# Kernel optimization log

Hardware: AMD Instinct MI355X
Metric: run time of the kernel (lower is better)

## Reference

```python
import jax, jax.numpy as jnp
import numpy as np

B, N, M, D, CD, H, DH = 2, 2048, 2048, 1024, 1024, 8, 64
INNER = H * DH  # 512
FFD = 4 * D
SCALE = DH ** -0.5


def _ln(x, g, b):
    mu = jnp.mean(x, axis=-1, keepdims=True)
    var = jnp.mean((x - mu) ** 2, axis=-1, keepdims=True)
    return (x - mu) * jax.lax.rsqrt(var + 1e-5) * g + b


def _ff(x, g, b, w1, b1, w2, b2):
    h = jax.nn.gelu(_ln(x, g, b) @ w1 + b1, approximate=False)
    return h @ w2 + b2


def setup_inputs() -> dict:
    key = jax.random.key(0)
    ks = jax.random.split(key, 16)
    s = 0.02
    return {
        'x': jax.random.normal(ks[0], (B, N, D), jnp.float32),
        'context': jax.random.normal(ks[1], (B, M, CD), jnp.float32),
        'mask': jnp.ones((B, N), bool),
        'context_mask': jnp.ones((B, M), bool),
        'ln_x_g': jnp.ones(D), 'ln_x_b': jnp.zeros(D),
        'ln_c_g': jnp.ones(CD), 'ln_c_b': jnp.zeros(CD),
        'W_qk': jax.random.normal(ks[2], (D, INNER)) * s,
        'W_v': jax.random.normal(ks[3], (D, INNER)) * s,
        'Wc_qk': jax.random.normal(ks[4], (CD, INNER)) * s,
        'Wc_v': jax.random.normal(ks[5], (CD, INNER)) * s,
        'W_out': jax.random.normal(ks[6], (INNER, D)) * s, 'b_out': jnp.zeros(D),
        'Wc_out': jax.random.normal(ks[7], (INNER, CD)) * s, 'bc_out': jnp.zeros(CD),
        'ff_g': jnp.ones(D), 'ff_b': jnp.zeros(D),
        'ff_w1': jax.random.normal(ks[8], (D, FFD)) * s, 'ff_b1': jnp.zeros(FFD),
        'ff_w2': jax.random.normal(ks[9], (FFD, D)) * s, 'ff_b2': jnp.zeros(D),
        'cff_g': jnp.ones(CD), 'cff_b': jnp.zeros(CD),
        'cff_w1': jax.random.normal(ks[10], (CD, FFD)) * s, 'cff_b1': jnp.zeros(FFD),
        'cff_w2': jax.random.normal(ks[11], (FFD, CD)) * s, 'cff_b2': jnp.zeros(CD),
    }


def reference(x, context, mask, context_mask,
              ln_x_g, ln_x_b, ln_c_g, ln_c_b,
              W_qk, W_v, Wc_qk, Wc_v, W_out, b_out, Wc_out, bc_out,
              ff_g, ff_b, ff_w1, ff_b1, ff_w2, ff_b2,
              cff_g, cff_b, cff_w1, cff_b1, cff_w2, cff_b2):
    # pre-norm bidirectional cross attention
    xn = _ln(x, ln_x_g, ln_x_b)
    cn = _ln(context, ln_c_g, ln_c_b)
    qk = (xn @ W_qk).reshape(B, N, H, DH)      # b i h d
    v = (xn @ W_v).reshape(B, N, H, DH)
    cqk = (cn @ Wc_qk).reshape(B, M, H, DH)    # b j h d
    cv = (cn @ Wc_v).reshape(B, M, H, DH)
    sim = jnp.einsum('bihd,bjhd->bhij', qk, cqk) * SCALE
    pair_mask = mask[:, None, :, None] & context_mask[:, None, None, :]
    big_neg = jnp.finfo(sim.dtype).max
    sim = jnp.where(pair_mask, sim, -big_neg)
    attn = jax.nn.softmax(sim, axis=-1)        # x attends over context (j)
    cattn = jax.nn.softmax(sim, axis=-2)       # context attends over x (i)
    out = jnp.einsum('bhij,bjhd->bihd', attn, cv).reshape(B, N, INNER)
    cout = jnp.einsum('bhij,bihd->bjhd', cattn, v).reshape(B, M, INNER)
    x = x + (out @ W_out + b_out)
    context = context + (cout @ Wc_out + bc_out)
    # dual pre-norm FFN residual
    x = _ff(x, ff_g, ff_b, ff_w1, ff_b1, ff_w2, ff_b2) + x
    context = _ff(context, cff_g, cff_b, cff_w1, cff_b1, cff_w2, cff_b2) + context
    return (x, context)
```

## Files before the change

kernel.cpp:

```cpp
#include <hip/hip_runtime.h>
#include <hip/hip_bf16.h>
#include <cmath>

typedef __hip_bfloat16 bf16;
typedef __attribute__((ext_vector_type(8))) short short8;
typedef __attribute__((ext_vector_type(4))) float f32x4;

#define B_     2
#define N_     2048
#define M_     2048
#define D_     1024
#define H_     8
#define DH_    64
#define INNER_ 512
#define FFD_   4096
#define ROWS   4096

__device__ __forceinline__ float b2f(bf16 x){ return __bfloat162float(x); }
__device__ __forceinline__ bf16  f2b(float x){ return __float2bfloat16(x); }
__device__ __forceinline__ float s2f(short s){
    unsigned u = ((unsigned)(unsigned short)s) << 16;
    float f; __builtin_memcpy(&f, &u, 4); return f;
}
__device__ __forceinline__ short f2s(float f){
    bf16 b = __float2bfloat16(f);
    short s; __builtin_memcpy(&s, &b, 2); return s;
}
__device__ __forceinline__ float ldx(const void* p, size_t i, bool isb){
    return isb ? __bfloat162float(((const bf16*)p)[i]) : ((const float*)p)[i];
}
__device__ __forceinline__ void stx(void* p, size_t i, float v, bool isb){
    if (isb) ((bf16*)p)[i] = f2b(v); else ((float*)p)[i] = v;
}
__device__ __forceinline__ void gld16(const bf16* g, bf16* l){
    __builtin_amdgcn_global_load_lds(
        (const __attribute__((address_space(1))) void*)g,
        (__attribute__((address_space(3))) void*)l, 16, 0, 0);
}
__device__ __forceinline__ short8 ds_read128(const bf16* p){
    unsigned a = (unsigned)(size_t)(const __attribute__((address_space(3))) bf16*)p;
    short8 r;
    asm volatile("ds_read_b128 %0, %1" : "=v"(r) : "v"(a));
    return r;
}

__global__ void probe_kernel(const void* ones, int* flag){
    unsigned w = *(const unsigned*)ones;
    *flag = (w == 0x3F803F80u) ? 1 : 0;
}

template<bool IN_EXT>
__global__ __launch_bounds__(256) void ln_kernel(const void* __restrict__ x,
    const void* __restrict__ g, const void* __restrict__ b,
    bf16* __restrict__ out, const int* __restrict__ flagp)
{
    const int C = 1024;
    bool f = (*flagp != 0);
    bool bx = IN_EXT ? f : true;
    size_t base = (size_t)blockIdx.x * C;
    int t = threadIdx.x;
    float v[4]; float s = 0.f;
#pragma unroll
    for (int q = 0; q < 4; q++){ v[q] = ldx(x, base + t + q*256, bx); s += v[q]; }
    __shared__ float red[256];
    red[t] = s; __syncthreads();
    for (int o = 128; o > 0; o >>= 1){ if (t < o) red[t] += red[t+o]; __syncthreads(); }
    float mu = red[0] * (1.0f/1024.0f);
    __syncthreads();
    s = 0.f;
#pragma unroll
    for (int q = 0; q < 4; q++){ float d = v[q]-mu; s += d*d; }
    red[t] = s; __syncthreads();
    for (int o = 128; o > 0; o >>= 1){ if (t < o) red[t] += red[t+o]; __syncthreads(); }
    float rstd = rsqrtf(red[0]*(1.0f/1024.0f) + 1e-5f);
    bf16* orow = out + base;
#pragma unroll
    for (int q = 0; q < 4; q++){
        int i = t + q*256;
        orow[i] = f2b((v[q]-mu)*rstd*ldx(g,i,f) + ldx(b,i,f));
    }
}

__global__ __launch_bounds__(256) void tcast_kernel(
    const void* __restrict__ in, bf16* __restrict__ out,
    int R, int Ccols, size_t ibs, size_t obs, int force_b16,
    const int* __restrict__ flagp)
{
    bool isb = force_b16 ? true : (*flagp != 0);
    __shared__ float T[32][33];
    size_t ib = (size_t)blockIdx.z * ibs, ob = (size_t)blockIdx.z * obs;
    int r0 = blockIdx.x * 32, c0 = blockIdx.y * 32;
    int tx = threadIdx.x & 31, ty = threadIdx.x >> 5;
#pragma unroll
    for (int rr = 0; rr < 32; rr += 8)
        T[ty + rr][tx] = ldx(in, ib + (size_t)(r0 + ty + rr) * Ccols + c0 + tx, isb);
    __syncthreads();
#pragma unroll
    for (int rr = 0; rr < 32; rr += 8)
        out[ob + (size_t)(c0 + ty + rr) * R + r0 + tx] = f2b(T[tx][ty + rr]);
}

template<int MODE, int EPI, int DP>
__global__ __launch_bounds__(256) void mfma_gemm(
    const bf16* __restrict__ A, const bf16* __restrict__ A2,
    const bf16* __restrict__ Bt,
    const void* __restrict__ bias, const void* __restrict__ bias2,
    const void* __restrict__ res,  const void* __restrict__ res2,
    void* __restrict__ C, void* __restrict__ C2,
    int K, int lda, int ldb, int ldc,
    size_t coff, size_t cstr, size_t roff, float scale, int bh0,
    int azdiv, size_t astr, size_t bstr, int zsplit,
    const int* __restrict__ flagp)
{
    __shared__ __align__(16) bf16 As[DP][128*32];
    __shared__ __align__(16) bf16 Bs[DP][128*32];
    const int t = threadIdx.x;
    const int wave = t >> 6, lane = t & 63;
    const int quad = lane >> 4, l16 = lane & 15;
    const int z = blockIdx.z;

    const bf16* Ab; const bf16* Bb;
    const void* biasp = bias; const void* resp = res; void* Cp = C;
    size_t cbase;
    if (MODE == 1){
        int bh = bh0 + z, b = bh >> 3, h = bh & 7;
        Ab = A + (size_t)b * N_ * lda + h * DH_ + (size_t)blockIdx.y * 128 * lda;
        Bb = Bt + (size_t)b * M_ * ldb + h * DH_ + (size_t)blockIdx.x * 128 * ldb;
        cbase = coff + (size_t)z * N_ * M_;
    } else {
        const bf16* Ause = A;
        if (z >= zsplit){
            if (A2)    Ause  = A2;
            if (bias2) biasp = bias2;
            if (res2)  resp  = res2;
            if (C2)    Cp    = C2;
        }
        Ab = Ause + (size_t)(z / azdiv) * astr + (size_t)blockIdx.y * 128 * lda;
        Bb = Bt + (size_t)z * bstr + (size_t)blockIdx.x * 128 * ldb;
        cbase = coff + (size_t)z * cstr;
    }

    const int c1 = t, c2 = t + 256;
    const int r1 = c1 >> 2, q1 = ((c1 & 3) - (r1 >> 1)) & 3;
    const int r2 = c2 >> 2, q2 = ((c2 & 3) - (r2 >> 1)) & 3;
    const bf16* ga1 = Ab + (size_t)r1 * lda + q1 * 8;
    const bf16* ga2 = Ab + (size_t)r2 * lda + q2 * 8;
    const bf16* gb1 = Bb + (size_t)r1 * ldb + q1 * 8;
    const bf16* gb2 = Bb + (size_t)r2 * ldb + q2 * 8;
    const int la1 = (wave * 64) * 8;
    const int la2 = (256 + wave * 64) * 8;
    const int moff = (wave & 1) * 64, noff = (wave >> 1) * 64;

    auto stage = [&](int d, int k0){
        gld16(ga1 + k0, &As[d][la1]);
        gld16(ga2 + k0, &As[d][la2]);
        gld16(gb1 + k0, &Bs[d][la1]);
        gld16(gb2 + k0, &Bs[d][la2]);
    };

    f32x4 acc[4][4];
#pragma unroll
    for (int mi = 0; mi < 4; mi++)
#pragma unroll
        for (int ni = 0; ni < 4; ni++)
#pragma unroll
            for (int r = 0; r < 4; r++) acc[mi][ni][r] = 0.f;

    const int nt = K >> 5;
    for (int d = 0; d < DP - 1; ++d)
        if (d < nt) stage(d, d * 32);

    for (int tt = 0; tt < nt; ++tt){
        if (tt + DP - 1 < nt) stage((tt + DP - 1) % DP, (tt + DP - 1) * 32);
        int rem = nt - 1 - tt;
        int lv  = rem < DP - 1 ? rem : DP - 1;
        if      (lv >= 3) asm volatile("s_waitcnt vmcnt(12)" ::: "memory");
        else if (lv == 2) asm volatile("s_waitcnt vmcnt(8)"  ::: "memory");
        else if (lv == 1) asm volatile("s_waitcnt vmcnt(4)"  ::: "memory");
        else              asm volatile("s_waitcnt vmcnt(0)"  ::: "memory");
        __builtin_amdgcn_s_barrier();
        const bf16* Al = As[tt % DP];
        const bf16* Bl = Bs[tt % DP];
        short8 af[4], bf8[4];
#pragma unroll
        for (int mi = 0; mi < 4; mi++){
            int rr = moff + mi*16 + l16;
            int qp = (quad + (rr >> 1)) & 3;
            af[mi] = ds_read128(Al + ((size_t)rr*4 + qp)*8);
        }
#pragma unroll
        for (int ni = 0; ni < 4; ni++){
            int rr = noff + ni*16 + l16;
            int qp = (quad + (rr >> 1)) & 3;
            bf8[ni] = ds_read128(Bl + ((size_t)rr*4 + qp)*8);
        }
        asm volatile("s_waitcnt lgkmcnt(0)" ::: "memory");
        __builtin_amdgcn_sched_barrier(0);
        __builtin_amdgcn_s_setprio(1);
#pragma unroll
        for (int mi = 0; mi < 4; mi++)
#pragma unroll
            for (int ni = 0; ni < 4; ni++)
                acc[mi][ni] = __builtin_amdgcn_mfma_f32_16x16x32_bf16(
                    af[mi], bf8[ni], acc[mi][ni], 0, 0, 0);
        __builtin_amdgcn_s_setprio(0);
        __builtin_amdgcn_s_barrier();
    }

    bool f = false;
    if (EPI >= 1) f = (*flagp != 0);
    const int mb = blockIdx.y * 128, nb = blockIdx.x * 128;
#pragma unroll
    for (int ni = 0; ni < 4; ni++){
        int n = nb + noff + ni*16 + l16;
        float bv = (EPI >= 1) ? ldx(biasp, n, f) : 0.0f;
#pragma unroll
        for (int mi = 0; mi < 4; mi++){
#pragma unroll
            for (int r = 0; r < 4; r++){
                int m = mb + moff + mi*16 + quad*4 + r;
                float val = acc[mi][ni][r] * scale + bv;
                if (EPI == 2) val = 0.5f*val*(1.0f + erff(val*0.70710678118f));
                size_t idx = (size_t)m * ldc + n;
                if (EPI == 3) val += ldx(resp, roff + idx, f);
                if (EPI == 4) val += b2f(((const bf16*)resp)[roff + idx]);
                if (EPI == 4) stx(Cp, cbase + idx, val, f);
                else ((bf16*)Cp)[cbase + idx] = f2b(val);
            }
        }
    }
}

__global__ __launch_bounds__(256) void flash_attn(
    const bf16* __restrict__ qk, const bf16* __restrict__ cqk,
    const bf16* __restrict__ vT, const bf16* __restrict__ cvT,
    bf16* __restrict__ aout, bf16* __restrict__ acout)
{
    __shared__ __align__(16) bf16 QP[64*72];
    __shared__ __align__(16) bf16 Ks[64*72];
    __shared__ __align__(16) bf16 Vs[64*72];
    const int t = threadIdx.x;
    const int wave = t >> 6, lane = t & 63, quad = lane >> 4, l16 = lane & 15;
    const int z = blockIdx.y;
    const int dir = z >> 4, bh = z & 15, b = bh >> 3, h = bh & 7;
    const bf16 *Qg, *Kg, *Vg; bf16* Og;
    if (dir == 0){ Qg = qk;  Kg = cqk; Vg = cvT; Og = aout;  }
    else         { Qg = cqk; Kg = qk;  Vg = vT;  Og = acout; }
    const int i0 = blockIdx.x * 64;
    const bf16* Qb = Qg + ((size_t)b*2048 + i0)*INNER_ + h*DH_;
    const bf16* Kb = Kg + (size_t)b*2048*INNER_ + h*DH_;
    const bf16* Vb = Vg + ((size_t)b*INNER_ + h*DH_)*2048;

    for (int c = t; c < 64*8; c += 256){
        int r = c >> 3, jc = c & 7;
        short8 raw = *(const short8*)(Qb + (size_t)r*INNER_ + jc*8);
        short8 s;
#pragma unroll
        for (int q = 0; q < 8; q++) s[q] = f2s(s2f(raw[q]) * 0.125f);
        *(short8*)(QP + r*72 + jc*8) = s;
    }
    __syncthreads();
    const int moff = wave * 16;
    short8 qf[2];
#pragma unroll
    for (int ks = 0; ks < 2; ks++){
        int rr = moff + l16;
        qf[ks] = *(const short8*)(QP + rr*72 + ks*32 + quad*8);
    }
    __syncthreads();

    f32x4 O[4];
    float mrow[4], lrow[4];
#pragma unroll
    for (int nd = 0; nd < 4; nd++)
#pragma unroll
        for (int r = 0; r < 4; r++) O[nd][r] = 0.f;
#pragma unroll
    for (int r = 0; r < 4; r++){ mrow[r] = -1e30f; lrow[r] = 0.f; }

    for (int j0 = 0; j0 < 2048; j0 += 64){
        for (int c = t; c < 64*8; c += 256){
            int r = c >> 3, jc = c & 7;
            short8 kraw = *(const short8*)(Kb + (size_t)(j0 + r)*INNER_ + jc*8);
            *(short8*)(Ks + r*72 + jc*8) = kraw;
            short8 vraw = *(const short8*)(Vb + (size_t)r*2048 + j0 + jc*8);
            *(short8*)(Vs + r*72 + jc*8) = vraw;
        }
        __syncthreads();
        f32x4 S[4];
#pragma unroll
        for (int ni = 0; ni < 4; ni++)
#pragma unroll
            for (int r = 0; r < 4; r++) S[ni][r] = 0.f;
#pragma unroll
        for (int ks = 0; ks < 2; ks++){
            short8 kf[4];
#pragma unroll
            for (int ni = 0; ni < 4; ni++){
                int rr = ni*16 + l16;
                kf[ni] = *(const short8*)(Ks + rr*72 + ks*32 + quad*8);
            }
#pragma unroll
            for (int ni = 0; ni < 4; ni++)
                S[ni] = __builtin_amdgcn_mfma_f32_16x16x32_bf16(
                    qf[ks], kf[ni], S[ni], 0, 0, 0);
        }
        float al[4];
#pragma unroll
        for (int r = 0; r < 4; r++){
            float rm = fmaxf(fmaxf(S[0][r], S[1][r]), fmaxf(S[2][r], S[3][r]));
#pragma unroll
            for (int d = 1; d < 16; d <<= 1)
                rm = fmaxf(rm, __shfl_xor(rm, d, 64));
            float mn = fmaxf(mrow[r], rm);
            al[r] = __expf(mrow[r] - mn);
            mrow[r] = mn;
        }
#pragma unroll
        for (int r = 0; r < 4; r++){
            float rs = 0.f;
#pragma unroll
            for (int ni = 0; ni < 4; ni++){
                float pv = __expf(S[ni][r] - mrow[r]);
                S[ni][r] = pv; rs += pv;
            }
#pragma unroll
            for (int d = 1; d < 16; d <<= 1)
                rs += __shfl_xor(rs, d, 64);
            lrow[r] = lrow[r]*al[r] + rs;
        }
#pragma unroll
        for (int nd = 0; nd < 4; nd++)
#pragma unroll
            for (int r = 0; r < 4; r++) O[nd][r] *= al[r];
#pragma unroll
        for (int ni = 0; ni < 4; ni++)
#pragma unroll
            for (int r = 0; r < 4; r++){
                int row = moff + quad*4 + r;
                QP[row*72 + ni*16 + l16] = f2b(S[ni][r]);
            }
        __syncthreads();
#pragma unroll
        for (int ks = 0; ks < 2; ks++){
            short8 pf, vf[4];
            {
                int rr = moff + l16;
                pf = *(const short8*)(QP + rr*72 + ks*32 + quad*8);
            }
#pragma unroll
            for (int nd = 0; nd < 4; nd++){
                int rr = nd*16 + l16;
                vf[nd] = *(const short8*)(Vs + rr*72 + ks*32 + quad*8);
            }
#pragma unroll
            for (int nd = 0; nd < 4; nd++)
                O[nd] = __builtin_amdgcn_mfma_f32_16x16x32_bf16(
                    pf, vf[nd], O[nd], 0, 0, 0);
        }
        __syncthreads();
    }
#pragma unroll
    for (int r = 0; r < 4; r++){
        float inv = 1.0f / lrow[r];
        int row = i0 + moff + quad*4 + r;
#pragma unroll
        for (int nd = 0; nd < 4; nd++){
            int d = nd*16 + l16;
            Og[((size_t)b*2048 + row)*INNER_ + h*DH_ + d] = f2b(O[nd][r] * inv);
        }
    }
}

extern "C" void kernel_launch(void* const* d_in, const int* in_sizes, int n_in,
                              void* d_out, int out_size, void* d_ws, size_t ws_size,
                              hipStream_t stream)
{
    const void* x      = d_in[0];
    const void* ctx    = d_in[1];
    const void* ln_x_g = d_in[4];
    const void* ln_x_b = d_in[5];
    const void* ln_c_g = d_in[6];
    const void* ln_c_b = d_in[7];
    const void* W_qk   = d_in[8];
    const void* W_v    = d_in[9];
    const void* Wc_qk  = d_in[10];
    const void* Wc_v   = d_in[11];
    const void* W_out  = d_in[12];
    const void* b_out  = d_in[13];
    const void* Wc_out = d_in[14];
    const void* bc_out = d_in[15];
    const void* ff_g   = d_in[16];
    const void* ff_b   = d_in[17];
    const void* ff_w1  = d_in[18];
    const void* ff_b1  = d_in[19];
    const void* ff_w2  = d_in[20];
    const void* ff_b2  = d_in[21];
    const void* cff_g  = d_in[22];
    const void* cff_b  = d_in[23];
    const void* cff_w1 = d_in[24];
    const void* cff_b1 = d_in[25];
    const void* cff_w2 = d_in[26];
    const void* cff_b2 = d_in[27];
    (void)in_sizes; (void)n_in; (void)out_size;

    const size_t MB = 1024ull*1024;
    char* p = (char*)d_ws;
    int*  flag = (int*)p;  p += 256;
    bf16* xn   = (bf16*)p; p += 8*MB;
    bf16* cn   = (bf16*)p; p += 8*MB;
    bf16* xmid = (bf16*)p; p += 8*MB;
    bf16* cmid = (bf16*)p; p += 8*MB;
    bf16* Wqk_t  = (bf16*)p; p += 1*MB;
    bf16* Wv_t   = (bf16*)p; p += 1*MB;
    bf16* Wcqk_t = (bf16*)p; p += 1*MB;
    bf16* Wcv_t  = (bf16*)p; p += 1*MB;
    bf16* Wout_t = (bf16*)p; p += 1*MB;
    bf16* Wcout_t= (bf16*)p; p += 1*MB;
    bf16* ffw1_t = (bf16*)p; p += 8*MB;
    bf16* ffw2_t = (bf16*)p; p += 8*MB;
    bf16* cffw1_t= (bf16*)p; p += 8*MB;
    bf16* cffw2_t= (bf16*)p; p += 8*MB;
    char* R = p; p += 32*MB;
    bf16* qk    = (bf16*)(R +  0*MB);
    bf16* vv    = (bf16*)(R +  4*MB);
    bf16* cqk   = (bf16*)(R +  8*MB);
    bf16* cv    = (bf16*)(R + 12*MB);
    bf16* aout  = (bf16*)(R + 16*MB);
    bf16* acout = (bf16*)(R + 20*MB);
    bf16* vT    = (bf16*)(R + 24*MB);
    bf16* cvT   = (bf16*)(R + 28*MB);
    bf16* hbuf  = (bf16*)R;
    p = (char*)(((size_t)p + 255) & ~(size_t)255);
    size_t fixed = (size_t)(p - (char*)d_ws);
    bf16* hbuf2 = (bf16*)p;
    bool batched_ffn = (ws_size >= fixed + 32*MB);

    probe_kernel<<<1, 1, 0, stream>>>(ln_x_g, flag);

    auto TC = [&](const void* in, bf16* o, int Rr, int Cc){
        tcast_kernel<<<dim3(Rr/32, Cc/32, 1), 256, 0, stream>>>(in, o, Rr, Cc, 0, 0, 0, flag);
    };
    TC(W_qk,   Wqk_t,  1024, 512);
    TC(W_v,    Wv_t,   1024, 512);
    TC(Wc_qk,  Wcqk_t, 1024, 512);
    TC(Wc_v,   Wcv_t,  1024, 512);
    TC(W_out,  Wout_t,  512, 1024);
    TC(Wc_out, Wcout_t, 512, 1024);
    TC(ff_w1,  ffw1_t, 1024, 4096);
    TC(ff_w2,  ffw2_t, 4096, 1024);
    TC(cff_w1, cffw1_t,1024, 4096);
    TC(cff_w2, cffw2_t,4096, 1024);

    ln_kernel<true><<<ROWS, 256, 0, stream>>>(x,   ln_x_g, ln_x_b, xn, flag);
    ln_kernel<true><<<ROWS, 256, 0, stream>>>(ctx, ln_c_g, ln_c_b, cn, flag);

    mfma_gemm<2,0,4><<<dim3(4,32,4), 256, 0, stream>>>(
        xn, nullptr, Wqk_t, nullptr, nullptr, nullptr, nullptr, qk, nullptr,
        1024, 1024, 1024, 512, 0, (size_t)ROWS*INNER_, 0, 1.f, 0,
        2, (size_t)(cn - xn), (size_t)(Wv_t - Wqk_t), 4, flag);

    tcast_kernel<<<dim3(64,16,2), 256, 0, stream>>>(vv, vT, 2048, 512,
        (size_t)N_*INNER_, (size_t)N_*INNER_, 1, flag);
    tcast_kernel<<<dim3(64,16,2), 256, 0, stream>>>(cv, cvT, 2048, 512,
        (size_t)M_*INNER_, (size_t)M_*INNER_, 1, flag);

    flash_attn<<<dim3(32, 32), 256, 0, stream>>>(qk, cqk, vT, cvT, aout, acout);

    mfma_gemm<2,3,4><<<dim3(8,32,2), 256, 0, stream>>>(
        aout, nullptr, Wout_t, b_out, bc_out, x, ctx, xmid, nullptr,
        512, 512, 512, 1024, 0, (size_t)ROWS*D_, 0, 1.f, 0,
        1, (size_t)(acout - aout), (size_t)(Wcout_t - Wout_t), 1, flag);

    if (batched_ffn){
        ln_kernel<false><<<ROWS, 256, 0, stream>>>(xmid, ff_g,  ff_b,  xn, flag);
        ln_kernel<false><<<ROWS, 256, 0, stream>>>(cmid, cff_g, cff_b, cn, flag);
        mfma_gemm<2,2,2><<<dim3(32,32,2), 256, 0, stream>>>(
            xn, nullptr, ffw1_t, ff_b1, cff_b1, nullptr, nullptr, hbuf, hbuf2,
            1024, 1024, 1024, 4096, 0, 0, 0, 1.f, 0,
            1, (size_t)(cn - xn), (size_t)(cffw1_t - ffw1_t), 1, flag);
        mfma_gemm<2,4,4><<<dim3(8,32,2), 256, 0, stream>>>(
            hbuf, hbuf2, ffw2_t, ff_b2, cff_b2, xmid, cmid, d_out, nullptr,
            4096, 4096, 4096, 1024, 0, (size_t)ROWS*D_, 0, 1.f, 0,
            1, 0, (size_t)(cffw2_t - ffw2_t), 1, flag);
    } else {
        ln_kernel<false><<<ROWS, 256, 0, stream>>>(xmid, ff_g, ff_b, xn, flag);
        mfma_gemm<2,2,2><<<dim3(32,32,1), 256, 0, stream>>>(
            xn, nullptr, ffw1_t, ff_b1, nullptr, nullptr, nullptr, hbuf, nullptr,
            1024, 1024, 1024, 4096, 0, 0, 0, 1.f, 0, 1, 0, 0, 1, flag);
        mfma_gemm<2,4,4><<<dim3(8,32,1), 256, 0, stream>>>(
            hbuf, nullptr, ffw2_t, ff_b2, nullptr, xmid, nullptr, d_out, nullptr,
            4096, 4096, 4096, 1024, 0, 0, 0, 1.f, 0, 1, 0, 0, 1, flag);
        ln_kernel<false><<<ROWS, 256, 0, stream>>>(cmid, cff_g, cff_b, cn, flag);
        mfma_gemm<2,2,2><<<dim3(32,32,1), 256, 0, stream>>>(
            cn, nullptr, cffw1_t, cff_b1, nullptr, nullptr, nullptr, hbuf, nullptr,
            1024, 1024, 1024, 4096, 0, 0, 0, 1.f, 0, 1, 0, 0, 1, flag);
        mfma_gemm<2,4,4><<<dim3(8,32,1), 256, 0, stream>>>(
            hbuf, nullptr, cffw2_t, cff_b2, nullptr, cmid, nullptr, d_out, nullptr,
            4096, 4096, 4096, 1024, (size_t)ROWS*D_, 0, 0, 1.f, 0, 1, 0, 0, 1, flag);
    }
}
```

Baseline: 653.0 us.

## Widen flash-attention KV tile to 128 and compute transposed scores

The flash attention kernel now processes 128 keys per iteration instead of 64 and computes S^T (K as the A operand), so each lane holds one query row. Row max and sum then need only two cross-lane shuffles instead of four per row. P is written to LDS as packed 4-element vectors per wave without a block-wide barrier before the PV MFMA, and one of the two barriers per iteration is removed. It uses more LDS and registers (S[8]), which may lower occupancy.

```diff
diff --git a/kernel.cpp b/kernel.cpp
--- a/kernel.cpp
+++ b/kernel.cpp
@@ -4,6 +4,7 @@
 
 typedef __hip_bfloat16 bf16;
 typedef __attribute__((ext_vector_type(8))) short short8;
+typedef __attribute__((ext_vector_type(4))) short short4g;
 typedef __attribute__((ext_vector_type(4))) float f32x4;
 
 #define B_     2
@@ -231,14 +232,16 @@
     }
 }
 
+#define KSTR 72
+#define PSTR 136
 __global__ __launch_bounds__(256) void flash_attn(
     const bf16* __restrict__ qk, const bf16* __restrict__ cqk,
     const bf16* __restrict__ vT, const bf16* __restrict__ cvT,
     bf16* __restrict__ aout, bf16* __restrict__ acout)
 {
-    __shared__ __align__(16) bf16 QP[64*72];
-    __shared__ __align__(16) bf16 Ks[64*72];
-    __shared__ __align__(16) bf16 Vs[64*72];
+    __shared__ __align__(16) bf16 QP[64*PSTR];
+    __shared__ __align__(16) bf16 Ks[128*KSTR];
+    __shared__ __align__(16) bf16 Vs[64*PSTR];
     const int t = threadIdx.x;
     const int wave = t >> 6, lane = t & 63, quad = lane >> 4, l16 = lane & 15;
     const int z = blockIdx.y;
@@ -257,117 +260,109 @@
         short8 s;
 #pragma unroll
         for (int q = 0; q < 8; q++) s[q] = f2s(s2f(raw[q]) * 0.125f);
-        *(short8*)(QP + r*72 + jc*8) = s;
+        *(short8*)(QP + r*PSTR + jc*8) = s;
     }
     __syncthreads();
     const int moff = wave * 16;
     short8 qf[2];
 #pragma unroll
-    for (int ks = 0; ks < 2; ks++){
-        int rr = moff + l16;
-        qf[ks] = *(const short8*)(QP + rr*72 + ks*32 + quad*8);
-    }
-    __syncthreads();
+    for (int ks = 0; ks < 2; ks++)
+        qf[ks] = *(const short8*)(QP + (moff + l16)*PSTR + ks*32 + quad*8);
 
     f32x4 O[4];
-    float mrow[4], lrow[4];
+    float mrow = -1e30f, lrow = 0.f;
 #pragma unroll
     for (int nd = 0; nd < 4; nd++)
 #pragma unroll
         for (int r = 0; r < 4; r++) O[nd][r] = 0.f;
-#pragma unroll
-    for (int r = 0; r < 4; r++){ mrow[r] = -1e30f; lrow[r] = 0.f; }
-
-    for (int j0 = 0; j0 < 2048; j0 += 64){
-        for (int c = t; c < 64*8; c += 256){
+
+    for (int j0 = 0; j0 < 2048; j0 += 128){
+        __syncthreads();
+        for (int c = t; c < 128*8; c += 256){
             int r = c >> 3, jc = c & 7;
             short8 kraw = *(const short8*)(Kb + (size_t)(j0 + r)*INNER_ + jc*8);
-            *(short8*)(Ks + r*72 + jc*8) = kraw;
+            *(short8*)(Ks + r*KSTR + jc*8) = kraw;
+        }
+        for (int c = t; c < 64*16; c += 256){
+            int r = c >> 4, jc = c & 15;
             short8 vraw = *(const short8*)(Vb + (size_t)r*2048 + j0 + jc*8);
-            *(short8*)(Vs + r*72 + jc*8) = vraw;
+            *(short8*)(Vs + r*PSTR + jc*8) = vraw;
         }
         __syncthreads();
-        f32x4 S[4];
-#pragma unroll
-        for (int ni = 0; ni < 4; ni++)
+        f32x4 S[8];
+#pragma unroll
+        for (int ni = 0; ni < 8; ni++)
 #pragma unroll
             for (int r = 0; r < 4; r++) S[ni][r] = 0.f;
 #pragma unroll
         for (int ks = 0; ks < 2; ks++){
-            short8 kf[4];
-#pragma unroll
-            for (int ni = 0; ni < 4; ni++){
-                int rr = ni*16 + l16;
-                kf[ni] = *(const short8*)(Ks + rr*72 + ks*32 + quad*8);
+#pragma unroll
+            for (int ni = 0; ni < 8; ni++){
+                short8 kf = *(const short8*)(Ks + (ni*16 + l16)*KSTR + ks*32 + quad*8);
+                S[ni] = __builtin_amdgcn_mfma_f32_16x16x32_bf16(
+                    kf, qf[ks], S[ni], 0, 0, 0);
             }
-#pragma unroll
-            for (int ni = 0; ni < 4; ni++)
-                S[ni] = __builtin_amdgcn_mfma_f32_16x16x32_bf16(
-                    qf[ks], kf[ni], S[ni], 0, 0, 0);
-        }
-        float al[4];
-#pragma unroll
-        for (int r = 0; r < 4; r++){
-            float rm = fmaxf(fmaxf(S[0][r], S[1][r]), fmaxf(S[2][r], S[3][r]));
-#pragma unroll
-            for (int d = 1; d < 16; d <<= 1)
-                rm = fmaxf(rm, __shfl_xor(rm, d, 64));
-            float mn = fmaxf(mrow[r], rm);
-            al[r] = __expf(mrow[r] - mn);
-            mrow[r] = mn;
-        }
-#pragma unroll
-        for (int r = 0; r < 4; r++){
-            float rs = 0.f;
-#pragma unroll
-            for (int ni = 0; ni < 4; ni++){
-                float pv = __expf(S[ni][r] - mrow[r]);
+        }
+        float rm = -1e30f;
+#pragma unroll
+        for (int ni = 0; ni < 8; ni++){
+            float a = fmaxf(S[ni][0], S[ni][1]);
+            float c2 = fmaxf(S[ni][2], S[ni][3]);
+            rm = fmaxf(rm, fmaxf(a, c2));
+        }
+        rm = fmaxf(rm, __shfl_xor(rm, 16, 64));
+        rm = fmaxf(rm, __shfl_xor(rm, 32, 64));
+        float mn = fmaxf(mrow, rm);
+        float al = __expf(mrow - mn);
+        mrow = mn;
+        float rs = 0.f;
+#pragma unroll
+        for (int ni = 0; ni < 8; ni++)
+#pragma unroll
+            for (int r = 0; r < 4; r++){
+                float pv = __expf(S[ni][r] - mn);
                 S[ni][r] = pv; rs += pv;
             }
-#pragma unroll
-            for (int d = 1; d < 16; d <<= 1)
-                rs += __shfl_xor(rs, d, 64);
-            lrow[r] = lrow[r]*al[r] + rs;
-        }
+        rs += __shfl_xor(rs, 16, 64);
+        rs += __shfl_xor(rs, 32, 64);
+        lrow = lrow*al + rs;
+        float alq[4];
+#pragma unroll
+        for (int r = 0; r < 4; r++) alq[r] = __shfl(al, quad*4 + r, 64);
 #pragma unroll
         for (int nd = 0; nd < 4; nd++)
 #pragma unroll
-            for (int r = 0; r < 4; r++) O[nd][r] *= al[r];
-#pragma unroll
-        for (int ni = 0; ni < 4; ni++)
-#pragma unroll
-            for (int r = 0; r < 4; r++){
-                int row = moff + quad*4 + r;
-                QP[row*72 + ni*16 + l16] = f2b(S[ni][r]);
-            }
-        __syncthreads();
-#pragma unroll
-        for (int ks = 0; ks < 2; ks++){
-            short8 pf, vf[4];
-            {
-                int rr = moff + l16;
-                pf = *(const short8*)(QP + rr*72 + ks*32 + quad*8);
-            }
-#pragma unroll
-            for (int nd = 0; nd < 4; nd++){
-                int rr = nd*16 + l16;
-                vf[nd] = *(const short8*)(Vs + rr*72 + ks*32 + quad*8);
-            }
+            for (int r = 0; r < 4; r++) O[nd][r] *= alq[r];
+#pragma unroll
+        for (int ni = 0; ni < 8; ni++){
+            short4g pk;
+#pragma unroll
+            for (int r = 0; r < 4; r++) pk[r] = f2s(S[ni][r]);
+            *(short4g*)(QP + (moff + l16)*PSTR + ni*16 + quad*4) = pk;
+        }
+#pragma unroll
+        for (int ks2 = 0; ks2 < 4; ks2++){
+            short8 pf = *(const short8*)(QP + (moff + l16)*PSTR + ks2*32 + quad*8);
+            short8 vf[4];
+#pragma unroll
+            for (int nd = 0; nd < 4; nd++)
+                vf[nd] = *(const short8*)(Vs + (nd*16 + l16)*PSTR + ks2*32 + quad*8);
 #pragma unroll
             for (int nd = 0; nd < 4; nd++)
                 O[nd] = __builtin_amdgcn_mfma_f32_16x16x32_bf16(
                     pf, vf[nd], O[nd], 0, 0, 0);
         }
-        __syncthreads();
-    }
+    }
+    float linv[4];
+#pragma unroll
+    for (int r = 0; r < 4; r++) linv[r] = 1.0f / __shfl(lrow, quad*4 + r, 64);
 #pragma unroll
     for (int r = 0; r < 4; r++){
-        float inv = 1.0f / lrow[r];
         int row = i0 + moff + quad*4 + r;
 #pragma unroll
         for (int nd = 0; nd < 4; nd++){
             int d = nd*16 + l16;
-            Og[((size_t)b*2048 + row)*INNER_ + h*DH_ + d] = f2b(O[nd][r] * inv);
+            Og[((size_t)b*2048 + row)*INNER_ + h*DH_ + d] = f2b(O[nd][r] * linv[r]);
         }
     }
 }
```

Result: no change. 655.7 us (+0.4%).
